# Optimization experiments

Measured on AMD Instinct MI355X. Metric: run time of the kernel, lower is better.

The kernel has to match this reference:

```python
import math
import jax, jax.numpy as jnp
import numpy as np

B, S, DIM, H = 16, 1024, 1024, 16
HD = DIM // H            # head_dim = 64
ROPE_DIM = HD // 2       # 32; per-axis rotary dim
FT = 32                  # ft_seq_len, FT*FT == S
PT = 16                  # pt_seq_len
THETA = 10000.0
EPS = 1e-6


def _rope_cos_sin():
    # freqs_for='lang'
    freqs = 1.0 / THETA ** (jnp.arange(0, ROPE_DIM, 2, dtype=jnp.float32) / ROPE_DIM)  # [ROPE_DIM//2]
    t = jnp.arange(FT, dtype=jnp.float32) / FT * PT                                    # [FT]
    fs = jnp.einsum('n,f->nf', t, freqs)                                               # [FT, ROPE_DIM//2]
    fs = jnp.repeat(fs, 2, axis=-1)                                                    # [FT, ROPE_DIM]
    fh = jnp.broadcast_to(fs[:, None, :], (FT, FT, ROPE_DIM))
    fw = jnp.broadcast_to(fs[None, :, :], (FT, FT, ROPE_DIM))
    f = jnp.concatenate([fh, fw], axis=-1).reshape(-1, 2 * ROPE_DIM)                   # [S, HD]
    return jnp.cos(f), jnp.sin(f)


def _rotate_half(x):
    x1, x2 = jnp.split(x, 2, axis=-1)
    return jnp.concatenate((-x2, x1), axis=-1)


def _rms_norm(x, w):
    xf = x.astype(jnp.float32)
    var = jnp.mean(jnp.square(xf), axis=-1, keepdims=True)
    return (w * (xf * jax.lax.rsqrt(var + EPS))).astype(x.dtype)


def setup_inputs() -> dict:
    key = jax.random.key(0)
    ks = jax.random.split(key, 4)
    sd = 1.0 / math.sqrt(DIM)
    return {
        'x': jax.random.normal(ks[0], (B, S, DIM), dtype=jnp.float32),
        'w_qkv': jax.random.normal(ks[1], (DIM, 3 * DIM), dtype=jnp.float32) * sd,
        'b_qkv': jnp.zeros((3 * DIM,), dtype=jnp.float32),
        'q_norm_w': jnp.ones((HD,), dtype=jnp.float32),
        'k_norm_w': jnp.ones((HD,), dtype=jnp.float32),
        'w_out': jax.random.normal(ks[2], (DIM, DIM), dtype=jnp.float32) * sd,
        'b_out': jnp.zeros((DIM,), dtype=jnp.float32),
    }


def reference(x, w_qkv, b_qkv, q_norm_w, k_norm_w, w_out, b_out):
    cos, sin = _rope_cos_sin()                    # [S, HD] each
    cos = cos[None, None].astype(x.dtype)
    sin = sin[None, None].astype(x.dtype)

    qkv = x @ w_qkv + b_qkv                       # [B,S,3*DIM]
    qkv = qkv.reshape(B, S, 3, H, HD).transpose(2, 0, 3, 1, 4)  # [3,B,H,S,HD]
    q, k, v = qkv[0], qkv[1], qkv[2]

    q = _rms_norm(q, q_norm_w)
    k = _rms_norm(k, k_norm_w)

    q = q * cos + _rotate_half(q) * sin
    k = k * cos + _rotate_half(k) * sin

    scale = 1.0 / math.sqrt(HD)
    logits = jnp.einsum('bhqd,bhkd->bhqk', q.astype(jnp.float32), k.astype(jnp.float32)) * scale
    attn = jax.nn.softmax(logits, axis=-1).astype(x.dtype)
    out = jnp.einsum('bhqk,bhkd->bhqd', attn, v)  # [B,H,S,HD]

    out = out.transpose(0, 2, 1, 3).reshape(B, S, DIM)
    return out @ w_out + b_out
```

## Files before the change

### kernel.cpp

```cpp
#include <hip/hip_runtime.h>
#include <cstdint>
#include <cstddef>

#define B_    16
#define S_    1024
#define DIM_  1024
#define H_    16
#define HD_   64
#define TDIM  3072

typedef unsigned short ushort_t;
typedef unsigned int   uint_t;
typedef __attribute__((ext_vector_type(8))) short s8v;
typedef __attribute__((ext_vector_type(4))) float f32x4;

__device__ __forceinline__ float b2f(ushort_t u) {
    union { uint_t i; float f; } t; t.i = (uint_t)u << 16; return t.f;
}
__device__ __forceinline__ ushort_t f2b(float f) {
    union { float f; uint_t i; } t; t.f = f;
    uint_t r = t.i + 0x7FFFu + ((t.i >> 16) & 1u);
    return (ushort_t)(r >> 16);
}
__device__ __forceinline__ uint_t cvt_pk_bf16(float a, float b) {
    uint_t r;
    asm("v_cvt_pk_bf16_f32 %0, %1, %2" : "=v"(r) : "v"(a), "v"(b));
    return r;
}

__device__ __forceinline__ f32x4 mfma_bf16(s8v a, s8v b, f32x4 c) {
    asm volatile("v_mfma_f32_16x16x32_bf16 %0, %1, %2, %0" : "+v"(c) : "v"(a), "v"(b));
    return c;
}

__device__ __forceinline__ void gload16(const void* g, void* l) {
    __builtin_amdgcn_global_load_lds(
        (const __attribute__((address_space(1))) uint_t*)g,
        (__attribute__((address_space(3))) uint_t*)l, 16, 0, 0);
}

__global__ __launch_bounds__(256) void f32_to_bf16_vec(const float* __restrict__ src,
                                                       short* __restrict__ dst, int n8) {
    int i = blockIdx.x * 256 + threadIdx.x;
    if (i < n8) {
        float4 a = *(const float4*)(src + (size_t)i * 8);
        float4 b = *(const float4*)(src + (size_t)i * 8 + 4);
        s8v t;
        t[0] = (short)f2b(a.x); t[1] = (short)f2b(a.y);
        t[2] = (short)f2b(a.z); t[3] = (short)f2b(a.w);
        t[4] = (short)f2b(b.x); t[5] = (short)f2b(b.y);
        t[6] = (short)f2b(b.z); t[7] = (short)f2b(b.w);
        *(s8v*)(dst + (size_t)i * 8) = t;
    }
}

__global__ __launch_bounds__(256) void rope_tables(float* __restrict__ cos_t,
                                                   float* __restrict__ sin_t) {
    int idx = blockIdx.x * 256 + threadIdx.x;
    int s = idx >> 6;
    int d = idx & 63;
    int pos = (d < 32) ? (s >> 5) : (s & 31);
    int i   = (d & 31) >> 1;
    float freq  = expf(-(float)i * 0.5756462732485115f);
    float angle = (float)pos * 0.5f * freq;
    cos_t[idx] = cosf(angle);
    sin_t[idx] = sinf(angle);
}

__global__ __launch_bounds__(256) void transpose_to_bf16(const float* __restrict__ Wsrc,
                                                         short* __restrict__ WT,
                                                         int K, int N) {
    __shared__ float t[32][33];
    int tx = threadIdx.x & 31, ty = threadIdx.x >> 5;
    int n0 = blockIdx.x * 32, k0 = blockIdx.y * 32;
#pragma unroll
    for (int i = 0; i < 4; ++i)
        t[ty + 8 * i][tx] = Wsrc[(size_t)(k0 + ty + 8 * i) * N + n0 + tx];
    __syncthreads();
#pragma unroll
    for (int i = 0; i < 4; ++i)
        WT[(size_t)(n0 + ty + 8 * i) * K + k0 + tx] = (short)f2b(t[tx][ty + 8 * i]);
}

template<typename CT, bool NORM>
__global__ __launch_bounds__(256) void gemm_glds(
        const short* __restrict__ A, const short* __restrict__ BT,
        const float* __restrict__ bias, CT* __restrict__ C,
        int M, int N, int K, int NX,
        const float* __restrict__ qw, const float* __restrict__ kw,
        const float* __restrict__ cos_t, const float* __restrict__ sin_t) {
    __shared__ short As[128 * 64];
    __shared__ short Bs[128 * 64];

    const int tid  = threadIdx.x;
    const int w    = tid >> 6;
    const int lane = tid & 63;
    const int l15  = lane & 15, lg = lane >> 4;

    const int nwg  = gridDim.x;
    const int cpx  = nwg >> 3;
    const int wgid = (blockIdx.x & 7) * cpx + (blockIdx.x >> 3);
    const int bx = wgid % NX, by = wgid / NX;
    const int m0 = by * 128, n0 = bx * 128;
    const int wr = (w >> 1) * 64, wc = (w & 1) * 64;

    const int srow = w * 32 + (lane >> 3);
    const int sk   = (lane & 7) * 8;

    f32x4 acc[4][4] = {};

    for (int k0 = 0; k0 < K; k0 += 64) {
        __syncthreads();
#pragma unroll
        for (int i = 0; i < 4; ++i) {
            int r = srow + i * 8;
            gload16(A  + (size_t)(m0 + r) * K + k0 + sk, &As[(w * 4 + i) * 512]);
            gload16(BT + (size_t)(n0 + r) * K + k0 + sk, &Bs[(w * 4 + i) * 512]);
        }
        __syncthreads();

#pragma unroll
        for (int kk = 0; kk < 2; ++kk) {
            s8v af[4], bf[4];
#pragma unroll
            for (int i = 0; i < 4; ++i) {
                af[i] = *(const s8v*)&As[(wr + 16 * i + l15) * 64 + kk * 32 + lg * 8];
                bf[i] = *(const s8v*)&Bs[(wc + 16 * i + l15) * 64 + kk * 32 + lg * 8];
            }
#pragma unroll
            for (int mi = 0; mi < 4; ++mi)
#pragma unroll
                for (int ni = 0; ni < 4; ++ni)
                    acc[mi][ni] = mfma_bf16(af[mi], bf[ni], acc[mi][ni]);
        }
    }

    if constexpr (NORM) {
        if (n0 + wc < 2048) {
            const float* nw = (n0 + wc < 1024) ? qw : kw;
            float wv[4], bv[4];
#pragma unroll
            for (int ni = 0; ni < 4; ++ni) {
                wv[ni] = nw[16 * ni + l15];
                bv[ni] = bias[n0 + wc + 16 * ni + l15];
            }
#pragma unroll
            for (int mi = 0; mi < 4; ++mi) {
#pragma unroll
                for (int r = 0; r < 4; ++r) {
                    int row = m0 + wr + 16 * mi + lg * 4 + r;
                    int s = row & (S_ - 1);
                    float v[4];
#pragma unroll
                    for (int ni = 0; ni < 4; ++ni) v[ni] = acc[mi][ni][r] + bv[ni];
                    float ss = v[0]*v[0] + v[1]*v[1] + v[2]*v[2] + v[3]*v[3];
                    ss += __shfl_xor(ss, 1);
                    ss += __shfl_xor(ss, 2);
                    ss += __shfl_xor(ss, 4);
                    ss += __shfl_xor(ss, 8);
                    float rms = rsqrtf(ss * (1.0f / 64.0f) + 1e-6f);
                    float xn[4];
#pragma unroll
                    for (int ni = 0; ni < 4; ++ni) xn[ni] = v[ni] * rms * wv[ni];
#pragma unroll
                    for (int ni = 0; ni < 4; ++ni) {
                        int d = 16 * ni + l15;
                        float c  = cos_t[s * 64 + d];
                        float sn = sin_t[s * 64 + d];
                        float rot = (ni < 2) ? -xn[ni + 2] : xn[ni - 2];
                        C[(size_t)row * N + n0 + wc + d] = (short)f2b(xn[ni] * c + rot * sn);
                    }
                }
            }
            return;
        }
    }
#pragma unroll
    for (int ni = 0; ni < 4; ++ni) {
        float bvv = bias[n0 + wc + 16 * ni + l15];
#pragma unroll
        for (int mi = 0; mi < 4; ++mi) {
#pragma unroll
            for (int r = 0; r < 4; ++r) {
                size_t row = (size_t)(m0 + wr + 16 * mi + lg * 4 + r);
                int    col = n0 + wc + 16 * ni + l15;
                float v = acc[mi][ni][r] + bvv;
                if constexpr (sizeof(CT) == 4) C[row * N + col] = v;
                else                           C[row * N + col] = (short)f2b(v);
            }
        }
    }
}

__global__ __launch_bounds__(256) void attn_mfma(const short* __restrict__ qkv,
                                                 short* __restrict__ attn) {
    __shared__ ushort_t Ks[64][72];
    __shared__ ushort_t Vt[64][72];
    __shared__ ushort_t Ps[4][32][72];

    const float SC  = 0.18033688011112042f;
    const float THR = 11.0f;

    const int tid  = threadIdx.x;
    const int w    = tid >> 6;
    const int lane = tid & 63;
    const int l15  = lane & 15, lg = lane >> 4;
    const int bh = blockIdx.y, b = bh >> 4, h = bh & 15;
    const int q0 = blockIdx.x * 128;

    const short* qbase = qkv + (size_t)b * S_ * TDIM + h * HD_;
    const short* kb = qbase + DIM_;
    const short* vb = qbase + 2 * DIM_;

    s8v qf[2][2];
#pragma unroll
    for (int mq = 0; mq < 2; ++mq)
#pragma unroll
        for (int kk = 0; kk < 2; ++kk)
            qf[mq][kk] = *(const s8v*)(qbase + (size_t)(q0 + w * 32 + mq * 16 + l15) * TDIM
                                       + kk * 32 + lg * 8);

    f32x4 of[2][4] = {};
    float m_s[2] = {-1e30f, -1e30f};
    float l_s[2] = {0.f, 0.f};

    const int kr   = tid >> 3;
    const int kp8  = (tid & 7) * 8;
    const int vkp  = tid >> 3;
    const int va   = tid & 7;
    const int vp8  = va * 8;
    const int vcol = (2 * vkp) ^ ((va & 3) << 4);

    s8v kA, kB, vA, vB;
    auto prefetch = [&](int kt) {
        const short* kbt = kb + (size_t)kt * 64 * TDIM;
        const short* vbt = vb + (size_t)kt * 64 * TDIM;
        kA = *(const s8v*)(kbt + (size_t)kr * TDIM + kp8);
        kB = *(const s8v*)(kbt + (size_t)(kr + 32) * TDIM + kp8);
        vA = *(const s8v*)(vbt + (size_t)(2 * vkp) * TDIM + vp8);
        vB = *(const s8v*)(vbt + (size_t)(2 * vkp + 1) * TDIM + vp8);
    };
    prefetch(0);

    for (int kt = 0; kt < 16; ++kt) {
        *(s8v*)&Ks[kr][kp8]      = kA;
        *(s8v*)&Ks[kr + 32][kp8] = kB;
#pragma unroll
        for (int j = 0; j < 8; ++j) {
            uint_t pk = (ushort_t)vA[j] | ((uint_t)(ushort_t)vB[j] << 16);
            *(uint_t*)&Vt[vp8 + j][vcol] = pk;
        }
        __syncthreads();

        if (kt < 15) prefetch(kt + 1);

        f32x4 st[4][2] = {};
        __builtin_amdgcn_s_setprio(1);
#pragma unroll
        for (int kk = 0; kk < 2; ++kk) {
            s8v kf[4];
#pragma unroll
            for (int nk = 0; nk < 4; ++nk)
                kf[nk] = *(const s8v*)&Ks[nk * 16 + l15][kk * 32 + lg * 8];
#pragma unroll
            for (int nk = 0; nk < 4; ++nk)
#pragma unroll
                for (int mq = 0; mq < 2; ++mq)
                    st[nk][mq] = mfma_bf16(kf[nk], qf[mq][kk], st[nk][mq]);
        }
        __builtin_amdgcn_s_setprio(0);

#pragma unroll
        for (int mq = 0; mq < 2; ++mq) {
            float mx = -1e30f;
#pragma unroll
            for (int nk = 0; nk < 4; ++nk)
#pragma unroll
                for (int r = 0; r < 4; ++r)
                    mx = fmaxf(mx, st[nk][mq][r]);
            mx = fmaxf(mx, __shfl_xor(mx, 16));
            mx = fmaxf(mx, __shfl_xor(mx, 32));
            float mxs = mx * SC;

            if (!__all(mxs <= m_s[mq] + THR)) {
                float mnew  = fmaxf(m_s[mq], mxs);
                float alpha = exp2f(m_s[mq] - mnew);
                m_s[mq] = mnew;
                l_s[mq] *= alpha;
                float a4[4];
#pragma unroll
                for (int r = 0; r < 4; ++r) a4[r] = __shfl(alpha, lg * 4 + r);
#pragma unroll
                for (int nd = 0; nd < 4; ++nd)
#pragma unroll
                    for (int r = 0; r < 4; ++r) of[mq][nd][r] *= a4[r];
            }

            float m = m_s[mq];
            float ls = 0.f;
#pragma unroll
            for (int nk = 0; nk < 4; ++nk) {
#pragma unroll
                for (int r = 0; r < 4; ++r) {
                    float p = exp2f(__builtin_fmaf(st[nk][mq][r], SC, -m));
                    st[nk][mq][r] = p;
                    ls += p;
                }
            }
            ls += __shfl_xor(ls, 16);
            ls += __shfl_xor(ls, 32);
            l_s[mq] += ls;

#pragma unroll
            for (int nk = 0; nk < 4; ++nk) {
                uint2 pk2;
                pk2.x = cvt_pk_bf16(st[nk][mq][0], st[nk][mq][1]);
                pk2.y = cvt_pk_bf16(st[nk][mq][2], st[nk][mq][3]);
                *(uint2*)&Ps[w][mq * 16 + l15][nk * 16 + lg * 4] = pk2;
            }
        }

        __builtin_amdgcn_s_setprio(1);
#pragma unroll
        for (int kk = 0; kk < 2; ++kk) {
            s8v pf[2], vf[4];
#pragma unroll
            for (int mq = 0; mq < 2; ++mq)
                pf[mq] = *(const s8v*)&Ps[w][mq * 16 + l15][kk * 32 + lg * 8];
#pragma unroll
            for (int nd = 0; nd < 4; ++nd) {
                int swz = (2 * nd + (l15 >> 3)) & 3;
                vf[nd] = *(const s8v*)&Vt[nd * 16 + l15][(kk * 32 + lg * 8) ^ (swz << 4)];
            }
#pragma unroll
            for (int mq = 0; mq < 2; ++mq)
#pragma unroll
                for (int nd = 0; nd < 4; ++nd)
                    of[mq][nd] = mfma_bf16(pf[mq], vf[nd], of[mq][nd]);
        }
        __builtin_amdgcn_s_setprio(0);
        __syncthreads();
    }

#pragma unroll
    for (int mq = 0; mq < 2; ++mq) {
        float rinv = 1.0f / l_s[mq];
        float iv[4];
#pragma unroll
        for (int r = 0; r < 4; ++r) iv[r] = __shfl(rinv, lg * 4 + r);
#pragma unroll
        for (int nd = 0; nd < 4; ++nd)
#pragma unroll
            for (int r = 0; r < 4; ++r) {
                int row = q0 + w * 32 + mq * 16 + lg * 4 + r;
                attn[((size_t)b * S_ + row) * DIM_ + h * HD_ + nd * 16 + l15] =
                    (short)f2b(of[mq][nd][r] * iv[r]);
            }
    }
}

extern "C" void kernel_launch(void* const* d_in, const int* in_sizes, int n_in,
                              void* d_out, int out_size, void* d_ws, size_t ws_size,
                              hipStream_t stream) {
    const float* x        = (const float*)d_in[0];
    const float* w_qkv    = (const float*)d_in[1];
    const float* b_qkv    = (const float*)d_in[2];
    const float* q_norm_w = (const float*)d_in[3];
    const float* k_norm_w = (const float*)d_in[4];
    const float* w_out    = (const float*)d_in[5];
    const float* b_out    = (const float*)d_in[6];
    float* out = (float*)d_out;

    const size_t OFF_QKV = 0;
    const size_t OFF_ATT = 100663296;
    const size_t OFF_XB  = OFF_ATT + 33554432;
    const size_t OFF_WQ  = OFF_XB + 33554432;
    const size_t OFF_WO  = OFF_WQ + 6291456;
    const size_t OFF_CT  = OFF_WO + 2097152;
    const size_t OFF_ST  = OFF_CT + 262144;
    const size_t NEED    = OFF_ST + 262144;

    if (ws_size < NEED) {
        hipMemsetAsync(d_out, 0, (size_t)out_size * sizeof(float), stream);
        return;
    }

    char* ws = (char*)d_ws;
    short* qkv   = (short*)(ws + OFF_QKV);
    short* attnb = (short*)(ws + OFF_ATT);
    short* xb    = (short*)(ws + OFF_XB);
    short* wqkvT = (short*)(ws + OFF_WQ);
    short* woutT = (short*)(ws + OFF_WO);
    float* cos_t = (float*)(ws + OFF_CT);
    float* sin_t = (float*)(ws + OFF_ST);

    rope_tables<<<dim3(256), dim3(256), 0, stream>>>(cos_t, sin_t);
    f32_to_bf16_vec<<<dim3(8192), dim3(256), 0, stream>>>(x, xb, 2097152);
    transpose_to_bf16<<<dim3(96, 32), dim3(256), 0, stream>>>(w_qkv, wqkvT, 1024, 3072);
    transpose_to_bf16<<<dim3(32, 32), dim3(256), 0, stream>>>(w_out, woutT, 1024, 1024);

    gemm_glds<short, true><<<dim3(3072), dim3(256), 0, stream>>>(
        xb, wqkvT, b_qkv, qkv, 16384, 3072, 1024, 24,
        q_norm_w, k_norm_w, cos_t, sin_t);

    attn_mfma<<<dim3(8, 256), dim3(256), 0, stream>>>(qkv, attnb);

    gemm_glds<float, false><<<dim3(1024), dim3(256), 0, stream>>>(
        attnb, woutT, b_out, out, 16384, 1024, 1024, 8,
        nullptr, nullptr, nullptr, nullptr);
}
```

Baseline: 346.1 us.

## Use 256x256 double-buffered 8-wave GEMM tiles and XCD-aware attention block mapping

Replaces the 128x128 single-buffered GEMM with a 512-thread, 256x256-tile kernel that double-buffers 32-wide K slices in LDS. The next tile's global-to-LDS loads are interleaved with the MFMA phases, and s_setprio is raised around the MFMAs. The aim is more operand reuse per LDS byte and hiding load latency behind compute. The attention grid is flattened and remapped so that each XCD handles a contiguous set of batch-heads, which should improve L2 locality for K/V. Risks include more register pressure from 32 accumulators per lane with launch_bounds(512,2), and fewer workgroups (256) for the output projection GEMM.

```diff
diff --git a/kernel.cpp b/kernel.cpp
--- a/kernel.cpp
+++ b/kernel.cpp
@@ -37,6 +37,15 @@
     __builtin_amdgcn_global_load_lds(
         (const __attribute__((address_space(1))) uint_t*)g,
         (__attribute__((address_space(3))) uint_t*)l, 16, 0, 0);
+}
+
+__device__ __forceinline__ void bar() {
+    asm volatile("" ::: "memory");
+    __builtin_amdgcn_s_barrier();
+    asm volatile("" ::: "memory");
+}
+__device__ __forceinline__ void wait_vm0() {
+    asm volatile("s_waitcnt vmcnt(0)" ::: "memory");
 }
 
 __global__ __launch_bounds__(256) void f32_to_bf16_vec(const float* __restrict__ src,
@@ -83,72 +92,104 @@
 }
 
 template<typename CT, bool NORM>
-__global__ __launch_bounds__(256) void gemm_glds(
+__global__ __launch_bounds__(512, 2) void gemm8(
         const short* __restrict__ A, const short* __restrict__ BT,
         const float* __restrict__ bias, CT* __restrict__ C,
         int M, int N, int K, int NX,
         const float* __restrict__ qw, const float* __restrict__ kw,
         const float* __restrict__ cos_t, const float* __restrict__ sin_t) {
-    __shared__ short As[128 * 64];
-    __shared__ short Bs[128 * 64];
+    __shared__ short As[2 * 256 * 32];
+    __shared__ short Bs[2 * 256 * 32];
 
     const int tid  = threadIdx.x;
     const int w    = tid >> 6;
     const int lane = tid & 63;
     const int l15  = lane & 15, lg = lane >> 4;
+    const int wm = w >> 2, wn = w & 3;
 
     const int nwg  = gridDim.x;
     const int cpx  = nwg >> 3;
     const int wgid = (blockIdx.x & 7) * cpx + (blockIdx.x >> 3);
     const int bx = wgid % NX, by = wgid / NX;
-    const int m0 = by * 128, n0 = bx * 128;
-    const int wr = (w >> 1) * 64, wc = (w & 1) * 64;
-
-    const int srow = w * 32 + (lane >> 3);
-    const int sk   = (lane & 7) * 8;
-
-    f32x4 acc[4][4] = {};
-
-    for (int k0 = 0; k0 < K; k0 += 64) {
-        __syncthreads();
-#pragma unroll
-        for (int i = 0; i < 4; ++i) {
-            int r = srow + i * 8;
-            gload16(A  + (size_t)(m0 + r) * K + k0 + sk, &As[(w * 4 + i) * 512]);
-            gload16(BT + (size_t)(n0 + r) * K + k0 + sk, &Bs[(w * 4 + i) * 512]);
-        }
-        __syncthreads();
-
-#pragma unroll
-        for (int kk = 0; kk < 2; ++kk) {
-            s8v af[4], bf[4];
-#pragma unroll
-            for (int i = 0; i < 4; ++i) {
-                af[i] = *(const s8v*)&As[(wr + 16 * i + l15) * 64 + kk * 32 + lg * 8];
-                bf[i] = *(const s8v*)&Bs[(wc + 16 * i + l15) * 64 + kk * 32 + lg * 8];
-            }
+    const int m0 = by * 256, n0 = bx * 256;
+
+    const int NT = K >> 5;
+
+    const int srow = w * 16 + (lane >> 2);
+    const int sk   = (lane & 3) * 8;
+
+    auto stageA = [&](int kt, int buf) {
+        int k0 = kt << 5;
+#pragma unroll
+        for (int h = 0; h < 2; ++h)
+            gload16(A + (size_t)(m0 + h * 128 + srow) * K + k0 + sk,
+                    &As[buf * 8192 + (h * 128 + w * 16) * 32]);
+    };
+    auto stageB = [&](int kt, int buf) {
+        int k0 = kt << 5;
+#pragma unroll
+        for (int h = 0; h < 2; ++h)
+            gload16(BT + (size_t)(n0 + h * 128 + srow) * K + k0 + sk,
+                    &Bs[buf * 8192 + (h * 128 + w * 16) * 32]);
+    };
+
+    stageA(0, 0);
+    stageB(0, 0);
+
+    f32x4 acc[8][4] = {};
+    s8v bf[4];
+
+    for (int kt = 0; kt < NT; ++kt) {
+        const int buf  = kt & 1;
+        const int nbuf = buf ^ 1;
+
+        wait_vm0();
+        bar();
+
+#pragma unroll
+        for (int ph = 0; ph < 2; ++ph) {
+            s8v af[4];
+#pragma unroll
+            for (int i = 0; i < 4; ++i)
+                af[i] = *(const s8v*)&As[buf * 8192 +
+                        (wm * 128 + ph * 64 + i * 16 + l15) * 32 + lg * 8];
+            if (ph == 0) {
+#pragma unroll
+                for (int i = 0; i < 4; ++i)
+                    bf[i] = *(const s8v*)&Bs[buf * 8192 +
+                            (wn * 64 + i * 16 + l15) * 32 + lg * 8];
+            }
+            if (kt + 1 < NT) {
+                if (ph == 0) stageA(kt + 1, nbuf);
+                else         stageB(kt + 1, nbuf);
+            }
+            bar();
+            __builtin_amdgcn_s_setprio(1);
 #pragma unroll
             for (int mi = 0; mi < 4; ++mi)
 #pragma unroll
                 for (int ni = 0; ni < 4; ++ni)
-                    acc[mi][ni] = mfma_bf16(af[mi], bf[ni], acc[mi][ni]);
-        }
-    }
-
+                    acc[ph * 4 + mi][ni] = mfma_bf16(af[mi], bf[ni], acc[ph * 4 + mi][ni]);
+            __builtin_amdgcn_s_setprio(0);
+            bar();
+        }
+    }
+
+    const int colbase = n0 + wn * 64;
     if constexpr (NORM) {
-        if (n0 + wc < 2048) {
-            const float* nw = (n0 + wc < 1024) ? qw : kw;
+        if (colbase < 2048) {
+            const float* nw = (colbase < 1024) ? qw : kw;
             float wv[4], bv[4];
 #pragma unroll
             for (int ni = 0; ni < 4; ++ni) {
                 wv[ni] = nw[16 * ni + l15];
-                bv[ni] = bias[n0 + wc + 16 * ni + l15];
-            }
-#pragma unroll
-            for (int mi = 0; mi < 4; ++mi) {
+                bv[ni] = bias[colbase + 16 * ni + l15];
+            }
+#pragma unroll
+            for (int mi = 0; mi < 8; ++mi) {
 #pragma unroll
                 for (int r = 0; r < 4; ++r) {
-                    int row = m0 + wr + 16 * mi + lg * 4 + r;
+                    int row = m0 + wm * 128 + mi * 16 + lg * 4 + r;
                     int s = row & (S_ - 1);
                     float v[4];
 #pragma unroll
@@ -168,7 +209,7 @@
                         float c  = cos_t[s * 64 + d];
                         float sn = sin_t[s * 64 + d];
                         float rot = (ni < 2) ? -xn[ni + 2] : xn[ni - 2];
-                        C[(size_t)row * N + n0 + wc + d] = (short)f2b(xn[ni] * c + rot * sn);
+                        C[(size_t)row * N + colbase + d] = (short)f2b(xn[ni] * c + rot * sn);
                     }
                 }
             }
@@ -177,13 +218,13 @@
     }
 #pragma unroll
     for (int ni = 0; ni < 4; ++ni) {
-        float bvv = bias[n0 + wc + 16 * ni + l15];
-#pragma unroll
-        for (int mi = 0; mi < 4; ++mi) {
+        float bvv = bias[colbase + 16 * ni + l15];
+#pragma unroll
+        for (int mi = 0; mi < 8; ++mi) {
 #pragma unroll
             for (int r = 0; r < 4; ++r) {
-                size_t row = (size_t)(m0 + wr + 16 * mi + lg * 4 + r);
-                int    col = n0 + wc + 16 * ni + l15;
+                size_t row = (size_t)(m0 + wm * 128 + mi * 16 + lg * 4 + r);
+                int    col = colbase + 16 * ni + l15;
                 float v = acc[mi][ni][r] + bvv;
                 if constexpr (sizeof(CT) == 4) C[row * N + col] = v;
                 else                           C[row * N + col] = (short)f2b(v);
@@ -205,8 +246,13 @@
     const int w    = tid >> 6;
     const int lane = tid & 63;
     const int l15  = lane & 15, lg = lane >> 4;
-    const int bh = blockIdx.y, b = bh >> 4, h = bh & 15;
-    const int q0 = blockIdx.x * 128;
+
+    const int bid = blockIdx.x;
+    const int xcd = bid & 7;
+    const int j   = bid >> 3;
+    const int bh  = xcd * 32 + (j & 31);
+    const int b   = bh >> 4, h = bh & 15;
+    const int q0  = (j >> 5) * 128;
 
     const short* qbase = qkv + (size_t)b * S_ * TDIM + h * HD_;
     const short* kb = qbase + DIM_;
@@ -246,9 +292,9 @@
         *(s8v*)&Ks[kr][kp8]      = kA;
         *(s8v*)&Ks[kr + 32][kp8] = kB;
 #pragma unroll
-        for (int j = 0; j < 8; ++j) {
-            uint_t pk = (ushort_t)vA[j] | ((uint_t)(ushort_t)vB[j] << 16);
-            *(uint_t*)&Vt[vp8 + j][vcol] = pk;
+        for (int jj = 0; jj < 8; ++jj) {
+            uint_t pk = (ushort_t)vA[jj] | ((uint_t)(ushort_t)vB[jj] << 16);
+            *(uint_t*)&Vt[vp8 + jj][vcol] = pk;
         }
         __syncthreads();
 
@@ -399,13 +445,13 @@
     transpose_to_bf16<<<dim3(96, 32), dim3(256), 0, stream>>>(w_qkv, wqkvT, 1024, 3072);
     transpose_to_bf16<<<dim3(32, 32), dim3(256), 0, stream>>>(w_out, woutT, 1024, 1024);
 
-    gemm_glds<short, true><<<dim3(3072), dim3(256), 0, stream>>>(
-        xb, wqkvT, b_qkv, qkv, 16384, 3072, 1024, 24,
+    gemm8<short, true><<<dim3(768), dim3(512), 0, stream>>>(
+        xb, wqkvT, b_qkv, qkv, 16384, 3072, 1024, 12,
         q_norm_w, k_norm_w, cos_t, sin_t);
 
-    attn_mfma<<<dim3(8, 256), dim3(256), 0, stream>>>(qkv, attnb);
-
-    gemm_glds<float, false><<<dim3(1024), dim3(256), 0, stream>>>(
-        attnb, woutT, b_out, out, 16384, 1024, 1024, 8,
+    attn_mfma<<<dim3(2048), dim3(256), 0, stream>>>(qkv, attnb);
+
+    gemm8<float, false><<<dim3(256), dim3(512), 0, stream>>>(
+        attnb, woutT, b_out, out, 16384, 1024, 1024, 4,
         nullptr, nullptr, nullptr, nullptr);
 }
```

Result: slower. 355.8 us (+2.8%).

## Switch attention to 32x32x16 MFMA with register P reuse and XCD-aware block mapping

Applied to the files above, without the earlier changes.

Rewrites the attention kernel to use 32x32x16 bf16 MFMAs, so each wave handles 32 query rows with one running max and sum per lane. The P tile is passed from the QK^T output layout into the PV operand layout through lane shuffles in registers, replacing the round trip through shared memory. The grid becomes 1D and is remapped so all q-tiles of a batch-head land on the same XCD, which should improve L2 reuse of K and V. The output is staged through LDS for coalesced 16-byte stores, at the cost of more register pressure from the 16-wide accumulators.

```diff
diff --git a/kernel.cpp b/kernel.cpp
--- a/kernel.cpp
+++ b/kernel.cpp
@@ -11,8 +11,9 @@
 
 typedef unsigned short ushort_t;
 typedef unsigned int   uint_t;
-typedef __attribute__((ext_vector_type(8))) short s8v;
-typedef __attribute__((ext_vector_type(4))) float f32x4;
+typedef __attribute__((ext_vector_type(8)))  short s8v;
+typedef __attribute__((ext_vector_type(4)))  float f32x4;
+typedef __attribute__((ext_vector_type(16))) float f32x16;
 
 __device__ __forceinline__ float b2f(ushort_t u) {
     union { uint_t i; float f; } t; t.i = (uint_t)u << 16; return t.f;
@@ -30,6 +31,10 @@
 
 __device__ __forceinline__ f32x4 mfma_bf16(s8v a, s8v b, f32x4 c) {
     asm volatile("v_mfma_f32_16x16x32_bf16 %0, %1, %2, %0" : "+v"(c) : "v"(a), "v"(b));
+    return c;
+}
+__device__ __forceinline__ f32x16 mfma32_bf16(s8v a, s8v b, f32x16 c) {
+    asm volatile("v_mfma_f32_32x32x16_bf16 %0, %1, %2, %0" : "+v"(c) : "v"(a), "v"(b));
     return c;
 }
 
@@ -194,9 +199,9 @@
 
 __global__ __launch_bounds__(256) void attn_mfma(const short* __restrict__ qkv,
                                                  short* __restrict__ attn) {
-    __shared__ ushort_t Ks[64][72];
-    __shared__ ushort_t Vt[64][72];
-    __shared__ ushort_t Ps[4][32][72];
+    __shared__ ushort_t pool[9216];
+    ushort_t* Ks = pool;
+    ushort_t* Vt = pool + 4608;
 
     const float SC  = 0.18033688011112042f;
     const float THR = 11.0f;
@@ -204,25 +209,26 @@
     const int tid  = threadIdx.x;
     const int w    = tid >> 6;
     const int lane = tid & 63;
-    const int l15  = lane & 15, lg = lane >> 4;
-    const int bh = blockIdx.y, b = bh >> 4, h = bh & 15;
-    const int q0 = blockIdx.x * 128;
+    const int l31  = lane & 31, l5 = lane >> 5;
+
+    const int bid = blockIdx.x;
+    const int xcd = bid & 7;
+    const int jj_ = bid >> 3;
+    const int bh  = xcd * 32 + (jj_ & 31);
+    const int b   = bh >> 4, h = bh & 15;
+    const int q0  = (jj_ >> 5) * 128;
 
     const short* qbase = qkv + (size_t)b * S_ * TDIM + h * HD_;
-    const short* kb = qbase + DIM_;
-    const short* vb = qbase + 2 * DIM_;
-
-    s8v qf[2][2];
-#pragma unroll
-    for (int mq = 0; mq < 2; ++mq)
-#pragma unroll
-        for (int kk = 0; kk < 2; ++kk)
-            qf[mq][kk] = *(const s8v*)(qbase + (size_t)(q0 + w * 32 + mq * 16 + l15) * TDIM
-                                       + kk * 32 + lg * 8);
-
-    f32x4 of[2][4] = {};
-    float m_s[2] = {-1e30f, -1e30f};
-    float l_s[2] = {0.f, 0.f};
+    const short* kb_ = qbase + DIM_;
+    const short* vb_ = qbase + 2 * DIM_;
+
+    s8v qf[4];
+#pragma unroll
+    for (int kc = 0; kc < 4; ++kc)
+        qf[kc] = *(const s8v*)(qbase + (size_t)(q0 + w * 32 + l31) * TDIM + kc * 16 + l5 * 8);
+
+    f32x16 of0 = {}, of1 = {};
+    float m_s = -1e30f, l_s = 0.f;
 
     const int kr   = tid >> 3;
     const int kp8  = (tid & 7) * 8;
@@ -230,11 +236,12 @@
     const int va   = tid & 7;
     const int vp8  = va * 8;
     const int vcol = (2 * vkp) ^ ((va & 3) << 4);
+    const int vsw  = ((l31 >> 3) & 3) << 4;
 
     s8v kA, kB, vA, vB;
     auto prefetch = [&](int kt) {
-        const short* kbt = kb + (size_t)kt * 64 * TDIM;
-        const short* vbt = vb + (size_t)kt * 64 * TDIM;
+        const short* kbt = kb_ + (size_t)kt * 64 * TDIM;
+        const short* vbt = vb_ + (size_t)kt * 64 * TDIM;
         kA = *(const s8v*)(kbt + (size_t)kr * TDIM + kp8);
         kB = *(const s8v*)(kbt + (size_t)(kr + 32) * TDIM + kp8);
         vA = *(const s8v*)(vbt + (size_t)(2 * vkp) * TDIM + vp8);
@@ -243,119 +250,103 @@
     prefetch(0);
 
     for (int kt = 0; kt < 16; ++kt) {
-        *(s8v*)&Ks[kr][kp8]      = kA;
-        *(s8v*)&Ks[kr + 32][kp8] = kB;
+        *(s8v*)&Ks[kr * 72 + kp8]        = kA;
+        *(s8v*)&Ks[(kr + 32) * 72 + kp8] = kB;
 #pragma unroll
         for (int j = 0; j < 8; ++j) {
             uint_t pk = (ushort_t)vA[j] | ((uint_t)(ushort_t)vB[j] << 16);
-            *(uint_t*)&Vt[vp8 + j][vcol] = pk;
+            *(uint_t*)&Vt[(vp8 + j) * 72 + vcol] = pk;
         }
         __syncthreads();
 
         if (kt < 15) prefetch(kt + 1);
 
-        f32x4 st[4][2] = {};
+        f32x16 st0 = {}, st1 = {};
         __builtin_amdgcn_s_setprio(1);
 #pragma unroll
-        for (int kk = 0; kk < 2; ++kk) {
-            s8v kf[4];
-#pragma unroll
-            for (int nk = 0; nk < 4; ++nk)
-                kf[nk] = *(const s8v*)&Ks[nk * 16 + l15][kk * 32 + lg * 8];
-#pragma unroll
-            for (int nk = 0; nk < 4; ++nk)
-#pragma unroll
-                for (int mq = 0; mq < 2; ++mq)
-                    st[nk][mq] = mfma_bf16(kf[nk], qf[mq][kk], st[nk][mq]);
+        for (int kc = 0; kc < 4; ++kc) {
+            s8v kf0 = *(const s8v*)&Ks[l31 * 72 + kc * 16 + l5 * 8];
+            s8v kf1 = *(const s8v*)&Ks[(32 + l31) * 72 + kc * 16 + l5 * 8];
+            st0 = mfma32_bf16(kf0, qf[kc], st0);
+            st1 = mfma32_bf16(kf1, qf[kc], st1);
         }
         __builtin_amdgcn_s_setprio(0);
 
-#pragma unroll
-        for (int mq = 0; mq < 2; ++mq) {
-            float mx = -1e30f;
-#pragma unroll
-            for (int nk = 0; nk < 4; ++nk)
-#pragma unroll
-                for (int r = 0; r < 4; ++r)
-                    mx = fmaxf(mx, st[nk][mq][r]);
-            mx = fmaxf(mx, __shfl_xor(mx, 16));
-            mx = fmaxf(mx, __shfl_xor(mx, 32));
-            float mxs = mx * SC;
-
-            if (!__all(mxs <= m_s[mq] + THR)) {
-                float mnew  = fmaxf(m_s[mq], mxs);
-                float alpha = exp2f(m_s[mq] - mnew);
-                m_s[mq] = mnew;
-                l_s[mq] *= alpha;
-                float a4[4];
-#pragma unroll
-                for (int r = 0; r < 4; ++r) a4[r] = __shfl(alpha, lg * 4 + r);
-#pragma unroll
-                for (int nd = 0; nd < 4; ++nd)
-#pragma unroll
-                    for (int r = 0; r < 4; ++r) of[mq][nd][r] *= a4[r];
+        float mx = -1e30f;
+#pragma unroll
+        for (int r = 0; r < 16; ++r)
+            mx = fmaxf(mx, fmaxf(st0[r], st1[r]));
+        mx = fmaxf(mx, __shfl_xor(mx, 32));
+        float mxs = mx * SC;
+
+        if (!__all(mxs <= m_s + THR)) {
+            float mnew  = fmaxf(m_s, mxs);
+            float alpha = exp2f(m_s - mnew);
+            m_s = mnew;
+            l_s *= alpha;
+#pragma unroll
+            for (int r = 0; r < 16; ++r) { of0[r] *= alpha; of1[r] *= alpha; }
+        }
+
+        float ls = 0.f;
+#pragma unroll
+        for (int r = 0; r < 16; ++r) {
+            float p0 = exp2f(__builtin_fmaf(st0[r], SC, -m_s));
+            float p1 = exp2f(__builtin_fmaf(st1[r], SC, -m_s));
+            st0[r] = p0; st1[r] = p1;
+            ls += p0 + ls * 0.0f + p1;
+        }
+        ls += __shfl_xor(ls, 32);
+        l_s += ls;
+
+        uint_t P20[8], P21[8];
+#pragma unroll
+        for (int i = 0; i < 8; ++i) {
+            P20[i] = cvt_pk_bf16(st0[2 * i], st0[2 * i + 1]);
+            P21[i] = cvt_pk_bf16(st1[2 * i], st1[2 * i + 1]);
+        }
+
+#pragma unroll
+        for (int kb = 0; kb < 2; ++kb) {
+            const uint_t* P2 = kb ? P21 : P20;
+#pragma unroll
+            for (int c = 0; c < 2; ++c) {
+                uint_t sw0 = __shfl_xor((int)P2[4 * c + 0], 32);
+                uint_t sw1 = __shfl_xor((int)P2[4 * c + 1], 32);
+                uint_t sw2 = __shfl_xor((int)P2[4 * c + 2], 32);
+                uint_t sw3 = __shfl_xor((int)P2[4 * c + 3], 32);
+                union { uint_t u[4]; s8v v; } pf;
+                pf.u[0] = l5 ? sw2           : P2[4 * c + 0];
+                pf.u[1] = l5 ? sw3           : P2[4 * c + 1];
+                pf.u[2] = l5 ? P2[4 * c + 2] : sw0;
+                pf.u[3] = l5 ? P2[4 * c + 3] : sw1;
+
+                int kcol = (kb * 32 + c * 16 + l5 * 8) ^ vsw;
+                s8v vf0 = *(const s8v*)&Vt[l31 * 72 + kcol];
+                s8v vf1 = *(const s8v*)&Vt[(32 + l31) * 72 + kcol];
+                __builtin_amdgcn_s_setprio(1);
+                of0 = mfma32_bf16(vf0, pf.v, of0);
+                of1 = mfma32_bf16(vf1, pf.v, of1);
+                __builtin_amdgcn_s_setprio(0);
             }
-
-            float m = m_s[mq];
-            float ls = 0.f;
-#pragma unroll
-            for (int nk = 0; nk < 4; ++nk) {
-#pragma unroll
-                for (int r = 0; r < 4; ++r) {
-                    float p = exp2f(__builtin_fmaf(st[nk][mq][r], SC, -m));
-                    st[nk][mq][r] = p;
-                    ls += p;
-                }
-            }
-            ls += __shfl_xor(ls, 16);
-            ls += __shfl_xor(ls, 32);
-            l_s[mq] += ls;
-
-#pragma unroll
-            for (int nk = 0; nk < 4; ++nk) {
-                uint2 pk2;
-                pk2.x = cvt_pk_bf16(st[nk][mq][0], st[nk][mq][1]);
-                pk2.y = cvt_pk_bf16(st[nk][mq][2], st[nk][mq][3]);
-                *(uint2*)&Ps[w][mq * 16 + l15][nk * 16 + lg * 4] = pk2;
-            }
-        }
-
-        __builtin_amdgcn_s_setprio(1);
-#pragma unroll
-        for (int kk = 0; kk < 2; ++kk) {
-            s8v pf[2], vf[4];
-#pragma unroll
-            for (int mq = 0; mq < 2; ++mq)
-                pf[mq] = *(const s8v*)&Ps[w][mq * 16 + l15][kk * 32 + lg * 8];
-#pragma unroll
-            for (int nd = 0; nd < 4; ++nd) {
-                int swz = (2 * nd + (l15 >> 3)) & 3;
-                vf[nd] = *(const s8v*)&Vt[nd * 16 + l15][(kk * 32 + lg * 8) ^ (swz << 4)];
-            }
-#pragma unroll
-            for (int mq = 0; mq < 2; ++mq)
-#pragma unroll
-                for (int nd = 0; nd < 4; ++nd)
-                    of[mq][nd] = mfma_bf16(pf[mq], vf[nd], of[mq][nd]);
-        }
-        __builtin_amdgcn_s_setprio(0);
+        }
         __syncthreads();
     }
 
-#pragma unroll
-    for (int mq = 0; mq < 2; ++mq) {
-        float rinv = 1.0f / l_s[mq];
-        float iv[4];
-#pragma unroll
-        for (int r = 0; r < 4; ++r) iv[r] = __shfl(rinv, lg * 4 + r);
-#pragma unroll
-        for (int nd = 0; nd < 4; ++nd)
-#pragma unroll
-            for (int r = 0; r < 4; ++r) {
-                int row = q0 + w * 32 + mq * 16 + lg * 4 + r;
-                attn[((size_t)b * S_ + row) * DIM_ + h * HD_ + nd * 16 + l15] =
-                    (short)f2b(of[mq][nd][r] * iv[r]);
-            }
+    float inv = 1.0f / l_s;
+    ushort_t* OL = pool + w * 2304;
+#pragma unroll
+    for (int r = 0; r < 16; ++r) {
+        int d = (r & 3) + 8 * (r >> 2) + 4 * l5;
+        OL[l31 * 72 + d]      = f2b(of0[r] * inv);
+        OL[l31 * 72 + 32 + d] = f2b(of1[r] * inv);
+    }
+#pragma unroll
+    for (int i = 0; i < 4; ++i) {
+        int idx = lane + i * 64;
+        int row = idx >> 3, ch = idx & 7;
+        *(s8v*)&attn[((size_t)b * S_ + q0 + w * 32 + row) * DIM_ + h * HD_ + ch * 8] =
+            *(const s8v*)&OL[row * 72 + ch * 8];
     }
 }
 
@@ -403,7 +394,7 @@
         xb, wqkvT, b_qkv, qkv, 16384, 3072, 1024, 24,
         q_norm_w, k_norm_w, cos_t, sin_t);
 
-    attn_mfma<<<dim3(8, 256), dim3(256), 0, stream>>>(qkv, attnb);
+    attn_mfma<<<dim3(2048), dim3(256), 0, stream>>>(qkv, attnb);
 
     gemm_glds<float, false><<<dim3(1024), dim3(256), 0, stream>>>(
         attnb, woutT, b_out, out, 16384, 1024, 1024, 8,
```

Measured after the change: 346.4 us. No clear change (+0.1%).
